# Kernel tuning notes

Hardware: AMD Instinct MI355X
Metric: run time of the kernel (lower is better)

The kernel has to match this reference:

```python
import jax, jax.numpy as jnp
import numpy as np
import math

N, S, R = 1, 128, 256
CM, CZ, C, MSA_H, PAIR_H, CTM, FF = 256, 128, 32, 8, 4, 128, 4
SCALE = 1.0 / math.sqrt(C)


def _ln(x, w, b):
    m = jnp.mean(x, -1, keepdims=True)
    v = jnp.var(x, -1, keepdims=True)
    return (x - m) / jnp.sqrt(v + 1e-5) * w + b


def _gated_attn(x, gate_w, qkv_w, out_w, head, bias=None):
    # x: [n, s, r, cin]; attention over r within each (n, s, head)
    n, s, r, _ = x.shape
    gate = jax.nn.sigmoid(x @ gate_w).reshape(n, s, r, head, C)
    qkv = (x @ qkv_w).reshape(n, s, r, 3, head, C)
    q, k, v = qkv[..., 0, :, :], qkv[..., 1, :, :], qkv[..., 2, :, :]
    sim = jax.nn.softmax(jnp.einsum('nsqhc,nskhc->nshqk', q, k) * SCALE, axis=-1)
    if bias is not None:
        sim = sim + bias  # NOTE: source adds bias AFTER softmax; kept faithful
    att = jnp.einsum('nshqk,nskhc->nsqhc', sim, v) * gate
    return att.reshape(n, s, r, head * C) @ out_w


def _tri_mul(x, n1w, n1b, n2w, n2b, p1, p2, p3, p4, p5, p6, incoming):
    xn = _ln(x, n1w, n1b)
    a = jax.nn.sigmoid(xn @ p1) * (xn @ p2)
    b = jax.nn.sigmoid(xn @ p3) * (xn @ p4)
    if incoming:
        p = jnp.einsum('nrsk,nrtk->nstk', a, b)
        g = jnp.swapaxes(jax.nn.sigmoid(xn @ p6), 1, 2)
    else:
        p = jnp.einsum('nsrk,ntrk->nstk', a, b)
        g = jax.nn.sigmoid(xn @ p6)
    return (_ln(p, n2w, n2b) @ p5) * g


def setup_inputs() -> dict:
    keys = iter(jax.random.split(jax.random.key(0), 80))

    def rn(shape, scale=0.02):
        return jax.random.normal(next(keys), shape, dtype=jnp.float32) * scale

    ones = lambda n: jnp.ones((n,), jnp.float32)
    zeros = lambda n: jnp.zeros((n,), jnp.float32)
    d = dict(
        msa_repr=rn((N, S, R, CM), 1.0),
        pair_repr=rn((N, R, R, CZ), 1.0),
        row_norm_m_w=ones(CM), row_norm_m_b=zeros(CM),
        row_norm_z_w=ones(CZ), row_norm_z_b=zeros(CZ),
        row_gate=rn((CM, MSA_H * C)), row_qkv=rn((CM, 3 * MSA_H * C)),
        row_out=rn((MSA_H * C, CM)), row_bias=rn((CZ, MSA_H)),
        col_norm_w=ones(CM), col_norm_b=zeros(CM),
        col_gate=rn((CM, MSA_H * C)), col_qkv=rn((CM, 3 * MSA_H * C)),
        col_out=rn((MSA_H * C, CM)),
        mt_norm_w=ones(CM), mt_norm_b=zeros(CM),
        mt_p1=rn((CM, FF * CM)), mt_p2=rn((FF * CM, CM)),
        outer_norm_w=ones(CM), outer_norm_b=zeros(CM),
        outer_p1=rn((CM, C)), outer_p2=rn((CM, C)), outer_out=rn((C * C, CZ)),
        tmo_n1_w=ones(CZ), tmo_n1_b=zeros(CZ), tmo_n2_w=ones(CTM), tmo_n2_b=zeros(CTM),
        tmo_p1=rn((CZ, CTM)), tmo_p2=rn((CZ, CTM)), tmo_p3=rn((CZ, CTM)), tmo_p4=rn((CZ, CTM)),
        tmo_p5=rn((CTM, CZ)), tmo_p6=rn((CZ, CZ)),
        tmi_n1_w=ones(CZ), tmi_n1_b=zeros(CZ), tmi_n2_w=ones(CTM), tmi_n2_b=zeros(CTM),
        tmi_p1=rn((CZ, CTM)), tmi_p2=rn((CZ, CTM)), tmi_p3=rn((CZ, CTM)), tmi_p4=rn((CZ, CTM)),
        tmi_p5=rn((CTM, CZ)), tmi_p6=rn((CZ, CZ)),
        tas_norm_w=ones(CZ), tas_norm_b=zeros(CZ),
        tas_gate=rn((CZ, PAIR_H * C)), tas_qkv=rn((CZ, 3 * PAIR_H * C)),
        tas_out=rn((PAIR_H * C, CZ)), tas_bias=rn((CZ, PAIR_H)),
        tae_norm_w=ones(CZ), tae_norm_b=zeros(CZ),
        tae_gate=rn((CZ, PAIR_H * C)), tae_qkv=rn((CZ, 3 * PAIR_H * C)),
        tae_out=rn((PAIR_H * C, CZ)), tae_bias=rn((CZ, PAIR_H)),
        pt_norm_w=ones(CZ), pt_norm_b=zeros(CZ),
        pt_p1=rn((CZ, FF * CZ)), pt_p2=rn((FF * CZ, CZ)),
    )
    return d


def reference(msa_repr, pair_repr, row_norm_m_w, row_norm_m_b, row_norm_z_w, row_norm_z_b, row_gate, row_qkv, row_out, row_bias, col_norm_w, col_norm_b, col_gate, col_qkv, col_out, mt_norm_w, mt_norm_b, mt_p1, mt_p2, outer_norm_w, outer_norm_b, outer_p1, outer_p2, outer_out, tmo_n1_w, tmo_n1_b, tmo_n2_w, tmo_n2_b, tmo_p1, tmo_p2, tmo_p3, tmo_p4, tmo_p5, tmo_p6, tmi_n1_w, tmi_n1_b, tmi_n2_w, tmi_n2_b, tmi_p1, tmi_p2, tmi_p3, tmi_p4, tmi_p5, tmi_p6, tas_norm_w, tas_norm_b, tas_gate, tas_qkv, tas_out, tas_bias, tae_norm_w, tae_norm_b, tae_gate, tae_qkv, tae_out, tae_bias, pt_norm_w, pt_norm_b, pt_p1, pt_p2):
    msa, pair = msa_repr, pair_repr
    # 1. MSA row attention with pair bias
    xm = _ln(msa, row_norm_m_w, row_norm_m_b)
    xz = _ln(pair, row_norm_z_w, row_norm_z_b)
    bias = jnp.transpose(xz @ row_bias, (0, 3, 1, 2))[:, None]  # [N,1,H,R,R]
    msa = msa + _gated_attn(xm, row_gate, row_qkv, row_out, MSA_H, bias)
    # 2. MSA column attention
    xm = _ln(msa, col_norm_w, col_norm_b)
    msa = msa + jnp.swapaxes(_gated_attn(jnp.swapaxes(xm, 1, 2), col_gate, col_qkv, col_out, MSA_H), 1, 2)
    # 3. MSA transition
    xm = _ln(msa, mt_norm_w, mt_norm_b)
    msa = msa + jax.nn.relu(xm @ mt_p1) @ mt_p2
    # 4. outer product mean (no division in source; sum over s)
    xm = _ln(msa, outer_norm_w, outer_norm_b)
    a = jnp.swapaxes(xm @ outer_p1, 1, 2)  # [n,r,s,c]
    b = jnp.swapaxes(xm @ outer_p2, 1, 2)  # [n,t,s,c]
    outer = jnp.einsum('nrsc,ntse->nrtce', a, b).reshape(a.shape[0], a.shape[1], b.shape[1], C * C)
    pair = pair + outer @ outer_out
    # 5/6. triangle multiplicative updates (outgoing then incoming)
    pair = pair + _tri_mul(pair, tmo_n1_w, tmo_n1_b, tmo_n2_w, tmo_n2_b, tmo_p1, tmo_p2, tmo_p3, tmo_p4, tmo_p5, tmo_p6, False)
    pair = pair + _tri_mul(pair, tmi_n1_w, tmi_n1_b, tmi_n2_w, tmi_n2_b, tmi_p1, tmi_p2, tmi_p3, tmi_p4, tmi_p5, tmi_p6, True)
    # 7. triangle attention (node start)
    xz = _ln(pair, tas_norm_w, tas_norm_b)
    bias = jnp.transpose(xz @ tas_bias, (0, 1, 3, 2))[:, :, :, None, :]  # [N,S,H,1,R]
    pair = pair + _gated_attn(xz, tas_gate, tas_qkv, tas_out, PAIR_H, bias)
    # 8. triangle attention (node end): transpose residue axes
    xz = jnp.swapaxes(_ln(pair, tae_norm_w, tae_norm_b), 1, 2)
    bias = jnp.transpose(xz @ tae_bias, (0, 1, 3, 2))[:, :, :, None, :]
    pair = pair + jnp.swapaxes(_gated_attn(xz, tae_gate, tae_qkv, tae_out, PAIR_H, bias), 1, 2)
    # 9. pair transition
    xz = _ln(pair, pt_norm_w, pt_norm_b)
    pair = pair + jax.nn.relu(xz @ pt_p1) @ pt_p2
    return msa, pair
```

## Files before the change

kernel.cpp:

```cpp
#include <hip/hip_runtime.h>
#include <hip/hip_bf16.h>
#include <stdint.h>

typedef __hip_bfloat16 bf16;
typedef __attribute__((ext_vector_type(4))) int   i32x4;
typedef __attribute__((ext_vector_type(4))) float f32x4;


__device__ __forceinline__ float toF(float x){ return x; }
__device__ __forceinline__ float toF(bf16 x){ return __bfloat162float(x); }
__device__ __forceinline__ bf16  toB(float x){ return __float2bfloat16(x); }

__device__ __forceinline__ void gload16(const bf16* g, bf16* l){
    __builtin_amdgcn_global_load_lds((const __attribute__((address_space(1))) void*)g,
                                     (__attribute__((address_space(3))) void*)l, 16, 0, 0);
}

#define NW_IN 58
struct WStage {
    const void* src[NW_IN];
    int off[NW_IN];
    int K[NW_IN], N[NW_IN];
};
__global__ __launch_bounds__(256) void cvt_all_k(WStage t, bf16* __restrict__ base,
                                                 const uint32_t* __restrict__ probe){
    bool isbf = (probe[0] == 0x3F803F80u);
    const int wi = blockIdx.y;
    const void* in = t.src[wi];
    bf16* out = base + t.off[wi];
    const int K = t.K[wi], N = t.N[wi];
    const int total = K ? K*N : N;
    for (int i = blockIdx.x*256 + threadIdx.x; i < total; i += gridDim.x*256){
        float v = isbf ? toF(((const bf16*)in)[i]) : ((const float*)in)[i];
        if (K){ int k = i / N, n = i - k*N; out[(size_t)n*K + k] = toB(v); }
        else    out[i] = toB(v);
    }
}
__global__ void in2f_k(const void* __restrict__ in, float* __restrict__ out, int n,
                       const uint32_t* __restrict__ probe){
    bool isbf = (probe[0] == 0x3F803F80u);
    int i = blockIdx.x*256 + threadIdx.x;
    if (i < n) out[i] = isbf ? toF(((const bf16*)in)[i]) : ((const float*)in)[i];
}

template<typename T>
__global__ void ln_k(const T* __restrict__ x, const bf16* __restrict__ w, const bf16* __restrict__ b,
                     bf16* __restrict__ out, int D){
    int row = blockIdx.x, c = threadIdx.x;
    float v = toF(x[(size_t)row*D + c]);
    float s1 = v, s2 = v*v;
    #pragma unroll
    for (int o=32;o>0;o>>=1){ s1 += __shfl_down(s1,o); s2 += __shfl_down(s2,o); }
    __shared__ float r1[4], r2[4];
    int lane = c & 63, wid = c >> 6;
    if (lane==0){ r1[wid]=s1; r2[wid]=s2; }
    __syncthreads();
    int nw = blockDim.x >> 6;
    float m=0.f, q=0.f;
    for (int i=0;i<nw;i++){ m+=r1[i]; q+=r2[i]; }
    m /= (float)D; q = q/(float)D - m*m;
    float inv = rsqrtf(q + 1e-5f);
    out[(size_t)row*D + c] = toB((v-m)*inv*toF(w[c]) + toF(b[c]));
}

template<int MODE, int HN>
__global__ __launch_bounds__(256) void bproj_k(const bf16* __restrict__ xz, const bf16* __restrict__ Wb,
                                               float* __restrict__ outb){
    __shared__ float WbS[128*HN];
    const int i = blockIdx.x, t = threadIdx.x;
    for (int idx = t; idx < 128*HN; idx += 256) WbS[idx] = toF(Wb[idx]);
    __syncthreads();
    const bf16* row = xz + ((size_t)i*256 + t)*128;
    float d[HN] = {};
    #pragma unroll 4
    for (int c8 = 0; c8 < 16; ++c8){
        uint4 v = *(const uint4*)(row + c8*8);
        bf16 tmp[8]; *(uint4*)tmp = v;
        #pragma unroll
        for (int u=0;u<8;u++){
            float x = toF(tmp[u]);
            #pragma unroll
            for (int h=0;h<HN;h++) d[h] += x * WbS[(c8*8+u)*HN + h];
        }
    }
    #pragma unroll
    for (int h=0;h<HN;h++){
        size_t idx = (MODE==0) ? ((size_t)h*65536 + (size_t)i*256 + t)
                   : (MODE==1) ? ((size_t)(i*HN+h)*256 + t)
                               : ((size_t)(t*HN+h)*256 + i);
        outb[idx] = d[h];
    }
}

template<int ACT, int MUL, int RES>
__global__ __launch_bounds__(256) void mgemm_k(const bf16* __restrict__ A, const bf16* __restrict__ Bt,
                                               bf16* __restrict__ C, float* __restrict__ Res,
                                               const bf16* __restrict__ Mul,
                                               int M, int N, int K, int lda, int ldbt, int ldc,
                                               int res_off, int gtrans){
    __shared__ alignas(16) bf16 As[128*32];
    __shared__ alignas(16) bf16 Bs[128*32];
    const int tid  = threadIdx.x;
    const int m0   = blockIdx.y << 7, n0 = blockIdx.x << 7;
    const int lane = tid & 63, w = tid >> 6;
    const int wr   = (w >> 1) << 6, wc = (w & 1) << 6;
    const int fr   = lane & 15, fq = lane >> 4;
    const int sr = tid >> 2, sc = (tid & 3) << 3;
    const bf16* ga = A  + (size_t)(m0 + sr)*lda  + sc;
    const bf16* gb = Bt + (size_t)(n0 + sr)*ldbt + sc;
    bf16* la = As + tid*8;
    bf16* lb = Bs + tid*8;
    const size_t gaS = (size_t)64*lda, gbS = (size_t)64*ldbt;

    f32x4 acc[4][4] = {};
    for (int k0=0; k0<K; k0+=32){
        gload16(ga, la);        gload16(ga + gaS, la + 2048);
        gload16(gb, lb);        gload16(gb + gbS, lb + 2048);
        ga += 32; gb += 32;
        __syncthreads();
        i32x4 af[4], bv[4];
        #pragma unroll
        for (int i=0;i<4;i++) af[i] = *(const i32x4*)(As + ((wr + i*16 + fr) << 5) + (fq << 3));
        #pragma unroll
        for (int j=0;j<4;j++) bv[j] = *(const i32x4*)(Bs + ((wc + j*16 + fr) << 5) + (fq << 3));
        #pragma unroll
        for (int i=0;i<4;i++)
            #pragma unroll
            for (int j=0;j<4;j++)
                asm("v_mfma_f32_16x16x32_bf16 %0, %1, %2, %0"
                    : "+v"(acc[i][j]) : "v"(af[i]), "v"(bv[j]));
        __syncthreads();
    }
    #pragma unroll
    for (int i=0;i<4;i++){
        const int mB = m0 + wr + i*16 + (fq << 2);
        #pragma unroll
        for (int j=0;j<4;j++){
            const int n = n0 + wc + j*16 + fr;
            #pragma unroll
            for (int r=0;r<4;r++){
                int m = mB + r;
                float x = acc[i][j][r];
                if (ACT==1) x = 1.f/(1.f + __expf(-x));
                else if (ACT==2) x = fmaxf(x, 0.f);
                if (MUL){
                    int mr = gtrans ? (((m & 255) << 8) | (m >> 8)) : m;
                    x *= toF(Mul[(size_t)mr*N + n]);
                }
                if (RES) Res[(size_t)(m + res_off)*N + n] += x;
                else     C[(size_t)m*ldc + n] = toB(x);
            }
        }
    }
}

template<int ACT, int MUL, int RES, int GATE>
__global__ __launch_bounds__(256) void sgemm_k(const bf16* __restrict__ A,
        const bf16* __restrict__ Bt1, const bf16* __restrict__ Bt2,
        bf16* __restrict__ C, float* __restrict__ Res, const bf16* __restrict__ Mul,
        int M, int lda, int ldbt, int ldc, int ldmul, int res_off, int gtrans){
    __shared__ alignas(16) bf16 Bs1[128*128];
    __shared__ alignas(16) bf16 Bs2[GATE ? 128*128 : 16];
    const int tid = threadIdx.x;
    for (int idx = tid; idx < 2048; idx += 256){
        int n = idx >> 4, cc = idx & 15;
        int sc = (cc ^ (n & 15)) << 3;
        *(uint4*)(Bs1 + n*128 + sc) = *(const uint4*)(Bt1 + (size_t)n*ldbt + (cc<<3));
        if (GATE)
            *(uint4*)(Bs2 + n*128 + sc) = *(const uint4*)(Bt2 + (size_t)n*ldbt + (cc<<3));
    }
    __syncthreads();
    const int lane = tid & 63, w = tid >> 6;
    const int fr = lane & 15, fq = lane >> 4;
    const int mb = blockIdx.x*128 + w*32;
    f32x4 acc[2][8] = {};
    f32x4 acc2[2][8] = {};
    #pragma unroll
    for (int k0=0;k0<4;k0++){
        i32x4 af[2];
        #pragma unroll
        for (int i=0;i<2;i++)
            af[i] = *(const i32x4*)(A + (size_t)(mb + i*16 + fr)*lda + k0*32 + fq*8);
        const int co = ((k0*4 + fq) ^ fr) << 3;
        #pragma unroll
        for (int j=0;j<8;j++){
            i32x4 bf1 = *(const i32x4*)(Bs1 + (j*16+fr)*128 + co);
            #pragma unroll
            for (int i=0;i<2;i++)
                asm("v_mfma_f32_16x16x32_bf16 %0, %1, %2, %0"
                    : "+v"(acc[i][j]) : "v"(af[i]), "v"(bf1));
            if (GATE){
                i32x4 bf2 = *(const i32x4*)(Bs2 + (j*16+fr)*128 + co);
                #pragma unroll
                for (int i=0;i<2;i++)
                    asm("v_mfma_f32_16x16x32_bf16 %0, %1, %2, %0"
                        : "+v"(acc2[i][j]) : "v"(af[i]), "v"(bf2));
            }
        }
    }
    #pragma unroll
    for (int i=0;i<2;i++){
        #pragma unroll
        for (int j=0;j<8;j++){
            const int n = j*16 + fr;
            #pragma unroll
            for (int r=0;r<4;r++){
                int m = mb + i*16 + (fq<<2) + r;
                float x = acc[i][j][r];
                if (GATE) x = acc2[i][j][r] / (1.f + __expf(-x));
                else if (ACT==1) x = 1.f/(1.f + __expf(-x));
                else if (ACT==2) x = fmaxf(x, 0.f);
                if (MUL){
                    int mr = gtrans ? (((m & 255) << 8) | (m >> 8)) : m;
                    x *= toF(Mul[(size_t)mr*ldmul + n]);
                }
                if (RES) Res[(size_t)(m + res_off)*128 + n] += x;
                else     C[(size_t)m*ldc + n] = toB(x);
            }
        }
    }
}

__global__ __launch_bounds__(256) void btrimul_k(const bf16* __restrict__ aT, const bf16* __restrict__ bT,
                                                 bf16* __restrict__ pT){
    __shared__ alignas(16) bf16 As[128*32];
    __shared__ alignas(16) bf16 Bs[128*32];
    const int tid  = threadIdx.x;
    const int m0   = blockIdx.y << 7, n0 = blockIdx.x << 7;
    const size_t zb = (size_t)blockIdx.z << 16;
    const int lane = tid & 63, w = tid >> 6;
    const int wr   = (w >> 1) << 6, wc = (w & 1) << 6;
    const int fr   = lane & 15, fq = lane >> 4;
    const int sr = tid >> 2, sc = (tid & 3) << 3;
    const bf16* ga = aT + zb + (size_t)(m0 + sr)*256 + sc;
    const bf16* gb = bT + zb + (size_t)(n0 + sr)*256 + sc;
    bf16* la = As + tid*8;
    bf16* lb = Bs + tid*8;
    const size_t gS = (size_t)64*256;

    f32x4 acc[4][4] = {};
    for (int k0=0; k0<256; k0+=32){
        gload16(ga, la);        gload16(ga + gS, la + 2048);
        gload16(gb, lb);        gload16(gb + gS, lb + 2048);
        ga += 32; gb += 32;
        __syncthreads();
        i32x4 af[4], bv[4];
        #pragma unroll
        for (int i=0;i<4;i++) af[i] = *(const i32x4*)(As + ((wr + i*16 + fr) << 5) + (fq << 3));
        #pragma unroll
        for (int j=0;j<4;j++) bv[j] = *(const i32x4*)(Bs + ((wc + j*16 + fr) << 5) + (fq << 3));
        #pragma unroll
        for (int i=0;i<4;i++)
            #pragma unroll
            for (int j=0;j<4;j++)
                asm("v_mfma_f32_16x16x32_bf16 %0, %1, %2, %0"
                    : "+v"(acc[i][j]) : "v"(af[i]), "v"(bv[j]));
        __syncthreads();
    }
    #pragma unroll
    for (int i=0;i<4;i++){
        const int mB = m0 + wr + i*16 + (fq << 2);
        #pragma unroll
        for (int j=0;j<4;j++){
            const int n = n0 + wc + j*16 + fr;
            #pragma unroll
            for (int r=0;r<4;r++)
                pT[zb + (size_t)(mB + r)*256 + n] = toB(acc[i][j][r]);
        }
    }
}

__global__ __launch_bounds__(256) void rc2k_k(const bf16* __restrict__ in, bf16* __restrict__ out, int swap){
    __shared__ uint16_t T[128][137];
    const int tt = blockIdx.x, tid = threadIdx.x;
    size_t base_pp, out_off; int ppstride;
    if (!swap){ base_pp = (size_t)tt*128;                  ppstride = 1;   out_off = (size_t)tt*128; }
    else      { int J = tt>>1, I0 = (tt&1)*128;
                base_pp = (size_t)I0*256 + J;              ppstride = 256; out_off = (size_t)J*256 + I0; }
    for (int it=0; it<8; ++it){
        int idx = tid + it*256;
        int r = idx >> 4, c8 = (idx & 15) << 3;
        uint4 v = *(const uint4*)(in + (base_pp + (size_t)r*ppstride)*128 + c8);
        uint16_t tmp[8]; *(uint4*)tmp = v;
        #pragma unroll
        for (int t=0;t<8;t++) T[r][c8+t] = tmp[t];
    }
    __syncthreads();
    for (int it=0; it<8; ++it){
        int idx = tid + it*256;
        int k = idx >> 4, r8 = (idx & 15) << 3;
        uint16_t tmp[8];
        #pragma unroll
        for (int t=0;t<8;t++) tmp[t] = T[r8+t][k];
        *(uint4*)(out + (size_t)k*65536 + out_off + r8) = *(uint4*)tmp;
    }
}
__global__ __launch_bounds__(256) void k2rc_k(const bf16* __restrict__ in, bf16* __restrict__ out){
    __shared__ uint16_t T[128][137];
    const int tt = blockIdx.x, tid = threadIdx.x;
    const size_t a0 = (size_t)tt*128;
    for (int it=0; it<8; ++it){
        int idx = tid + it*256;
        int k = idx >> 4, r8 = (idx & 15) << 3;
        uint4 v = *(const uint4*)(in + (size_t)k*65536 + a0 + r8);
        uint16_t tmp[8]; *(uint4*)tmp = v;
        #pragma unroll
        for (int t=0;t<8;t++) T[r8+t][k] = tmp[t];
    }
    __syncthreads();
    for (int it=0; it<8; ++it){
        int idx = tid + it*256;
        int r = idx >> 4, c8 = (idx & 15) << 3;
        uint16_t tmp[8];
        #pragma unroll
        for (int t=0;t<8;t++) tmp[t] = T[r][c8+t];
        *(uint4*)(out + (a0 + r)*128 + c8) = *(uint4*)tmp;
    }
}

template<int ACT, int MUL, int RES>
__global__ __launch_bounds__(256) void gemm_k(const bf16* __restrict__ A, const bf16* __restrict__ Bw,
                                              bf16* __restrict__ C, float* __restrict__ Res,
                                              const bf16* __restrict__ Mul,
                                              int M, int N, int K, int ldb, int res_off, int gtrans){
    __shared__ float As[64][33];
    __shared__ float Bs[32][65];
    int tid = threadIdx.x;
    int m0 = blockIdx.y*64, n0 = blockIdx.x*64;
    int tx = tid & 15, ty = tid >> 4;
    float acc[4][4] = {};
    for (int k0=0; k0<K; k0+=32){
        for (int i=tid; i<64*32; i+=256){
            int r = i>>5, cc = i&31;
            As[r][cc] = toF(A[(size_t)(m0+r)*K + k0 + cc]);
        }
        for (int i=tid; i<32*64; i+=256){
            int r = i>>6, cc = i&63; int col = n0+cc;
            Bs[r][cc] = (col < N) ? toF(Bw[(size_t)(k0+r)*ldb + col]) : 0.f;
        }
        __syncthreads();
        #pragma unroll 8
        for (int k=0;k<32;k++){
            float a4[4], b4[4];
            #pragma unroll
            for (int i=0;i<4;i++) a4[i] = As[ty*4+i][k];
            #pragma unroll
            for (int j=0;j<4;j++) b4[j] = Bs[k][tx*4+j];
            #pragma unroll
            for (int i=0;i<4;i++)
                #pragma unroll
                for (int j=0;j<4;j++) acc[i][j] += a4[i]*b4[j];
        }
        __syncthreads();
    }
    #pragma unroll
    for (int i=0;i<4;i++){
        int m = m0 + ty*4 + i;
        #pragma unroll
        for (int j=0;j<4;j++){
            int n = n0 + tx*4 + j;
            if (n >= N) continue;
            float x = acc[i][j];
            if (ACT==1) x = 1.f/(1.f + __expf(-x));
            else if (ACT==2) x = fmaxf(x, 0.f);
            if (MUL){
                int mr = gtrans ? (((m & 255) << 8) | (m >> 8)) : m;
                x *= toF(Mul[(size_t)mr*N + n]);
            }
            if (RES) Res[(size_t)(m + res_off)*N + n] += x;
            else     C[(size_t)m*N + n] = toB(x);
        }
    }
}

template<int BIAS, int L>
__global__ __launch_bounds__(256) void attn4_k(bf16* __restrict__ QO,
                                               const bf16* __restrict__ Kp, const bf16* __restrict__ Vp,
                                               const float* __restrict__ bias,
                                               int H, int GN, int sO, int sL){
    constexpr int MW  = L/4;
    constexpr int IFR = MW/16;
    constexpr int KC  = 32;
    constexpr int NCH = L/KC;
    constexpr int VP  = L + 8;
    __shared__ alignas(16) bf16 VT_lds[32*VP];
    __shared__ alignas(16) bf16 P_lds[L*40];
    __shared__ float red[8*32 + 32];
    const int o = blockIdx.y, h = blockIdx.x, tid = threadIdx.x;
    const int lane = tid & 63, w = tid >> 6;
    const int fr = lane & 15, fq = lane >> 4;

    for (int idx = tid; idx < L*4; idx += 256){
        int l = idx >> 2, c8 = (idx & 3) << 3;
        size_t p = (size_t)(o*sO + l*sL)*GN + h*32 + c8;
        uint4 vv = *(const uint4*)(Vp + p);
        bf16 tmp[8]; *(uint4*)tmp = vv;
        #pragma unroll
        for (int t=0;t<8;t++) VT_lds[(c8+t)*VP + l] = tmp[t];
    }
    __syncthreads();

    float* ObS = red + 256;
    if (BIAS == 2){
        int c = tid & 31, g = tid >> 5;
        const float* bp = bias + (size_t)(o*H + h)*256;
        float p = 0.f;
        for (int k = g*(L/8); k < (g+1)*(L/8); ++k)
            p += bp[k] * toF(VT_lds[c*VP + k]);
        red[g*32 + c] = p;
        __syncthreads();
        if (tid < 32){
            float s = 0.f;
            #pragma unroll
            for (int g2=0; g2<8; ++g2) s += red[g2*32 + tid];
            ObS[tid] = s;
        }
        __syncthreads();
    }

    i32x4 qf[IFR];
    #pragma unroll
    for (int i=0;i<IFR;i++){
        int q = w*MW + i*16 + fr;
        qf[i] = *(const i32x4*)(QO + (size_t)(o*sO + q*sL)*GN + h*32 + fq*8);
    }
    const bf16* kbase = Kp + (size_t)o*sO*GN + h*32 + fq*8 + (size_t)fr*sL*GN;
    const size_t kstep = (size_t)sL*GN;

    bf16* Pw = P_lds + w*MW*40;
    f32x4 accO[IFR][2] = {};
    f32x4 accB[IFR][2] = {};
    float lsum[IFR][4] = {};

    for (int ch=0; ch<NCH; ++ch){
        const int k0 = ch*KC;
        f32x4 sa[IFR][2] = {};
        i32x4 kf[2];
        #pragma unroll
        for (int j=0;j<2;j++) kf[j] = *(const i32x4*)(kbase + (size_t)(k0 + j*16)*kstep);
        #pragma unroll
        for (int i=0;i<IFR;i++)
            #pragma unroll
            for (int j=0;j<2;j++)
                asm("v_mfma_f32_16x16x32_bf16 %0, %1, %2, %0"
                    : "+v"(sa[i][j]) : "v"(qf[i]), "v"(kf[j]));
        #pragma unroll
        for (int i=0;i<IFR;i++)
            #pragma unroll
            for (int j=0;j<2;j++)
                #pragma unroll
                for (int r=0;r<4;r++){
                    float e = __expf(sa[i][j][r] * 0.17677669529663687f);
                    lsum[i][r] += e;
                    Pw[(i*16 + fq*4 + r)*40 + j*16 + fr] = toB(e);
                }
        i32x4 vf[2];
        #pragma unroll
        for (int j=0;j<2;j++) vf[j] = *(const i32x4*)(VT_lds + (j*16 + fr)*VP + k0 + fq*8);
        #pragma unroll
        for (int i=0;i<IFR;i++){
            i32x4 pa = *(const i32x4*)(Pw + (i*16 + fr)*40 + fq*8);
            #pragma unroll
            for (int j=0;j<2;j++)
                asm("v_mfma_f32_16x16x32_bf16 %0, %1, %2, %0"
                    : "+v"(accO[i][j]) : "v"(pa), "v"(vf[j]));
        }
        if (BIAS == 1){
            #pragma unroll
            for (int it=0; it<32; ++it){
                int q = it*2 + (lane>>5), kk = lane&31;
                Pw[q*40 + kk] = toB(bias[(size_t)h*65536 + (size_t)(w*MW + q)*256 + k0 + kk]);
            }
            #pragma unroll
            for (int i=0;i<IFR;i++){
                i32x4 pa = *(const i32x4*)(Pw + (i*16 + fr)*40 + fq*8);
                #pragma unroll
                for (int j=0;j<2;j++)
                    asm("v_mfma_f32_16x16x32_bf16 %0, %1, %2, %0"
                        : "+v"(accB[i][j]) : "v"(pa), "v"(vf[j]));
            }
        }
    }
    #pragma unroll
    for (int i=0;i<IFR;i++)
        #pragma unroll
        for (int r=0;r<4;r++){
            float s = lsum[i][r];
            s += __shfl_xor(s, 1); s += __shfl_xor(s, 2);
            s += __shfl_xor(s, 4); s += __shfl_xor(s, 8);
            lsum[i][r] = 1.f / s;
        }
    #pragma unroll
    for (int i=0;i<IFR;i++)
        #pragma unroll
        for (int j=0;j<2;j++)
            #pragma unroll
            for (int r=0;r<4;r++){
                int q = w*MW + i*16 + fq*4 + r;
                int c = j*16 + fr;
                float v = accO[i][j][r]*lsum[i][r];
                if (BIAS==1) v += accB[i][j][r];
                if (BIAS==2) v += ObS[c];
                QO[(size_t)(o*sO + q*sL)*GN + h*32 + c] = toB(v);
            }
}

__global__ void mulsig2_k(bf16* __restrict__ a, int n){
    int i = blockIdx.x*256 + threadIdx.x;
    if (i < n){
        int m = i >> 8, c = i & 255;
        size_t o = (size_t)m*768 + c;
        float sg = 1.f/(1.f + __expf(-toF(a[o + 256])));
        a[o] = toB(toF(a[o]) * sg);
    }
}

__global__ __launch_bounds__(256) void outer_k(const bf16* __restrict__ ap, const bf16* __restrict__ bp,
                                               bf16* __restrict__ outc, int r0){
    int t = blockIdx.x, rl = blockIdx.y, r = r0 + rl;
    __shared__ float As[128*32], Bs[128*32];
    for (int idx=threadIdx.x; idx<128*32; idx+=256){
        int s = idx>>5, c = idx&31;
        As[idx] = toF(ap[((size_t)s*256 + r)*32 + c]);
        Bs[idx] = toF(bp[((size_t)s*256 + t)*32 + c]);
    }
    __syncthreads();
    int ce0 = threadIdx.x*4;
    int c = ce0 >> 5, e0 = ce0 & 31;
    float acc[4] = {0.f,0.f,0.f,0.f};
    for (int s=0;s<128;s++){
        float av = As[s*32 + c];
        #pragma unroll
        for (int j=0;j<4;j++) acc[j] += av*Bs[s*32 + e0 + j];
    }
    size_t row = (size_t)rl*256 + t;
    #pragma unroll
    for (int j=0;j<4;j++) outc[row*1024 + ce0 + j] = toB(acc[j]);
}

static bool tshape(int i, int& K, int& N){
    switch(i){
        case 6: case 8: case 12: case 14: K=256; N=256;  return true;
        case 7: case 13:                  K=256; N=768;  return true;
        case 17:                          K=256; N=1024; return true;
        case 18:                          K=1024;N=256;  return true;
        case 23:                          K=1024;N=128;  return true;
        case 47: case 53:                 K=128; N=384;  return true;
        case 58:                          K=128; N=512;  return true;
        case 59:                          K=512; N=128;  return true;
        default:
            if ((i>=28&&i<=33)||(i>=38&&i<=43)||i==46||i==48||i==52||i==54){ K=128; N=128; return true; }
            return false;
    }
}

extern "C" void kernel_launch(void* const* d_in, const int* in_sizes, int n_in,
                              void* d_out, int out_size, void* d_ws, size_t ws_size,
                              hipStream_t stream){
    (void)n_in; (void)out_size; (void)ws_size;
    const int MSA_N  = 128*256*256;
    const int PAIR_N = 256*256*128;
    const uint32_t* probe = (const uint32_t*)d_in[2];

    char*  w     = (char*)d_ws;
    bf16*  wsts  = (bf16*)(w);
    float* biasF = (float*)(w + 4194304);
    bf16*  lnb   = (bf16*)(w + 6291456);
    bf16*  bufA  = (bf16*)(w + 23068672);
    bf16*  bufB  = (bf16*)(w + 39845888);
    bf16*  bufC  = (bf16*)(w + 56623104);

    float* msaF  = (float*)d_out;
    float* pairF = msaF + MSA_N;

    size_t woff[64]; { size_t acc = 0;
        for (int i=2;i<60;i++){ woff[i] = acc; acc += ((size_t)in_sizes[i] + 63) & ~(size_t)63; } }
    #define W(i) (wsts + woff[i])

    {
        WStage st;
        for (int i=2;i<60;i++){
            int tk, tn;
            st.src[i-2] = d_in[i];
            st.off[i-2] = (int)woff[i];
            if (tshape(i, tk, tn)){ st.K[i-2]=tk; st.N[i-2]=tn; }
            else                   { st.K[i-2]=0;  st.N[i-2]=in_sizes[i]; }
        }
        cvt_all_k<<<dim3(64, NW_IN),256,0,stream>>>(st, wsts, probe);
    }

    in2f_k<<<32768,256,0,stream>>>(d_in[0], msaF,  MSA_N,  probe);
    in2f_k<<<32768,256,0,stream>>>(d_in[1], pairF, PAIR_N, probe);

    ln_k<float><<<32768,256,0,stream>>>(msaF, W(2), W(3), lnb, 256);
    ln_k<float><<<65536,128,0,stream>>>(pairF, W(4), W(5), bufC, 128);
    bproj_k<0,8><<<256,256,0,stream>>>(bufC, W(9), biasF);
    mgemm_k<0,0,0><<<dim3(6,256),256,0,stream>>>(lnb, W(7), bufA, nullptr, nullptr,
                                                 32768,768,256, 256,256,768, 0,0);
    attn4_k<1,256><<<dim3(8,128),256,0,stream>>>(bufA, bufA+256, bufA+512, biasF, 8, 768, 256, 1);
    mgemm_k<0,0,0><<<dim3(2,256),256,0,stream>>>(lnb, W(6), bufA+256, nullptr, nullptr,
                                                 32768,256,256, 256,256,768, 0,0);
    mulsig2_k<<<32768,256,0,stream>>>(bufA, MSA_N);
    mgemm_k<0,0,1><<<dim3(2,256),256,0,stream>>>(bufA, W(8), nullptr, msaF, nullptr,
                                                 32768,256,256, 768,256,256, 0,0);

    ln_k<float><<<32768,256,0,stream>>>(msaF, W(10), W(11), lnb, 256);
    mgemm_k<0,0,0><<<dim3(6,256),256,0,stream>>>(lnb, W(13), bufA, nullptr, nullptr,
                                                 32768,768,256, 256,256,768, 0,0);
    attn4_k<0,128><<<dim3(8,256),256,0,stream>>>(bufA, bufA+256, bufA+512, nullptr, 8, 768, 1, 256);
    mgemm_k<0,0,0><<<dim3(2,256),256,0,stream>>>(lnb, W(12), bufA+256, nullptr, nullptr,
                                                 32768,256,256, 256,256,768, 0,0);
    mulsig2_k<<<32768,256,0,stream>>>(bufA, MSA_N);
    mgemm_k<0,0,1><<<dim3(2,256),256,0,stream>>>(bufA, W(14), nullptr, msaF, nullptr,
                                                 32768,256,256, 768,256,256, 0,0);

    ln_k<float><<<32768,256,0,stream>>>(msaF, W(15), W(16), lnb, 256);
    for (int ch=0; ch<4; ++ch){
        mgemm_k<2,0,0><<<dim3(2,256),256,0,stream>>>(lnb, W(17)+ch*65536, bufA, nullptr, nullptr,
                                                     32768,256,256, 256,256,256, 0,0);
        mgemm_k<0,0,1><<<dim3(2,256),256,0,stream>>>(bufA, W(18)+ch*256, nullptr, msaF, nullptr,
                                                     32768,256,256, 256,1024,256, 0,0);
    }

    ln_k<float><<<32768,256,0,stream>>>(msaF, W(19), W(20), lnb, 256);
    gemm_k<0,0,0><<<dim3(1,512),256,0,stream>>>(lnb, W(21), bufA, nullptr, nullptr, 32768,32,256, 32, 0,0);
    gemm_k<0,0,0><<<dim3(1,512),256,0,stream>>>(lnb, W(22), bufB, nullptr, nullptr, 32768,32,256, 32, 0,0);
    for (int ch=0; ch<8; ++ch){
        outer_k<<<dim3(256,32),256,0,stream>>>(bufA, bufB, lnb, ch*32);
        mgemm_k<0,0,1><<<dim3(1,64),256,0,stream>>>(lnb, W(23), nullptr, pairF, nullptr,
                                                    8192,128,1024, 1024,1024,128, ch*8192,0);
    }

    for (int tm=0; tm<2; ++tm){
        int o = tm ? 34 : 24;
        int inc = tm;
        ln_k<float><<<65536,128,0,stream>>>(pairF, W(o+0), W(o+1), lnb, 128);
        sgemm_k<0,0,0,1><<<512,256,0,stream>>>(lnb, W(o+4), W(o+5), bufA, nullptr, nullptr,
                                               65536, 128,128,128,0, 0,0);
        sgemm_k<0,0,0,1><<<512,256,0,stream>>>(lnb, W(o+6), W(o+7), bufB, nullptr, nullptr,
                                               65536, 128,128,128,0, 0,0);
        rc2k_k<<<512,256,0,stream>>>(bufA, bufC, inc);
        rc2k_k<<<512,256,0,stream>>>(bufB, bufA, inc);
        btrimul_k<<<dim3(2,2,128),256,0,stream>>>(bufC, bufA, bufB);
        k2rc_k<<<512,256,0,stream>>>(bufB, bufC);
        ln_k<bf16><<<65536,128,0,stream>>>(bufC, W(o+2), W(o+3), bufC, 128);
        sgemm_k<1,0,0,0><<<512,256,0,stream>>>(lnb, W(o+9), nullptr, bufA, nullptr, nullptr,
                                               65536, 128,128,128,0, 0,0);
        sgemm_k<0,1,1,0><<<512,256,0,stream>>>(bufC, W(o+8), nullptr, nullptr, pairF, bufA,
                                               65536, 128,128,0,128, 0, inc);
    }

    ln_k<float><<<65536,128,0,stream>>>(pairF, W(44), W(45), lnb, 128);
    bproj_k<1,4><<<256,256,0,stream>>>(lnb, W(49), biasF);
    mgemm_k<0,0,0><<<dim3(3,512),256,0,stream>>>(lnb, W(47), bufA, nullptr, nullptr,
                                                 65536,384,128, 128,128,384, 0,0);
    attn4_k<2,256><<<dim3(4,256),256,0,stream>>>(bufA, bufA+128, bufA+256, biasF, 4, 384, 256, 1);
    sgemm_k<1,1,0,0><<<512,256,0,stream>>>(lnb, W(46), nullptr, bufA+128, nullptr, bufA,
                                           65536, 128,128,384,384, 0,0);
    sgemm_k<0,0,1,0><<<512,256,0,stream>>>(bufA+128, W(48), nullptr, nullptr, pairF, nullptr,
                                           65536, 384,128,0,0, 0,0);
    ln_k<float><<<65536,128,0,stream>>>(pairF, W(50), W(51), lnb, 128);
    bproj_k<2,4><<<256,256,0,stream>>>(lnb, W(55), biasF);
    mgemm_k<0,0,0><<<dim3(3,512),256,0,stream>>>(lnb, W(53), bufA, nullptr, nullptr,
                                                 65536,384,128, 128,128,384, 0,0);
    attn4_k<2,256><<<dim3(4,256),256,0,stream>>>(bufA, bufA+128, bufA+256, biasF, 4, 384, 1, 256);
    sgemm_k<1,1,0,0><<<512,256,0,stream>>>(lnb, W(52), nullptr, bufA+128, nullptr, bufA,
                                           65536, 128,128,384,384, 0,0);
    sgemm_k<0,0,1,0><<<512,256,0,stream>>>(bufA+128, W(54), nullptr, nullptr, pairF, nullptr,
                                           65536, 384,128,0,0, 0,0);

    ln_k<float><<<65536,128,0,stream>>>(pairF, W(56), W(57), lnb, 128);
    for (int ch=0; ch<4; ++ch){
        sgemm_k<2,0,0,0><<<512,256,0,stream>>>(lnb, W(58)+ch*16384, nullptr, bufA, nullptr, nullptr,
                                               65536, 128,128,128,0, 0,0);
        sgemm_k<0,0,1,0><<<512,256,0,stream>>>(bufA, W(59)+ch*128, nullptr, nullptr, pairF, nullptr,
                                               65536, 128,512,0,0, 0,0);
    }
}
```

Baseline: 2.499 ms.

## Store QKV projections head-major so attention reads contiguous per-head slabs

```diff
diff --git a/kernel.cpp b/kernel.cpp
--- a/kernel.cpp
+++ b/kernel.cpp
@@ -92,12 +92,12 @@
     }
 }
 
-template<int ACT, int MUL, int RES>
+template<int ACT, int MUL, int RES, int HM>
 __global__ __launch_bounds__(256) void mgemm_k(const bf16* __restrict__ A, const bf16* __restrict__ Bt,
                                                bf16* __restrict__ C, float* __restrict__ Res,
                                                const bf16* __restrict__ Mul,
-                                               int M, int N, int K, int lda, int ldbt, int ldc,
-                                               int res_off, int gtrans){
+                                               int M, int N, int K, int lda, size_t astep,
+                                               int ldbt, size_t ldc, int res_off, int gtrans){
     __shared__ alignas(16) bf16 As[128*32];
     __shared__ alignas(16) bf16 Bs[128*32];
     const int tid  = threadIdx.x;
@@ -116,7 +116,7 @@
     for (int k0=0; k0<K; k0+=32){
         gload16(ga, la);        gload16(ga + gaS, la + 2048);
         gload16(gb, lb);        gload16(gb + gbS, lb + 2048);
-        ga += 32; gb += 32;
+        ga += astep; gb += 32;
         __syncthreads();
         i32x4 af[4], bv[4];
         #pragma unroll
@@ -148,17 +148,18 @@
                     x *= toF(Mul[(size_t)mr*N + n]);
                 }
                 if (RES) Res[(size_t)(m + res_off)*N + n] += x;
+                else if (HM) C[(size_t)(n>>5)*ldc + (size_t)m*32 + (n&31)] = toB(x);
                 else     C[(size_t)m*ldc + n] = toB(x);
             }
         }
     }
 }
 
-template<int ACT, int MUL, int RES, int GATE>
+template<int ACT, int MUL, int RES, int GATE, int MHM>
 __global__ __launch_bounds__(256) void sgemm_k(const bf16* __restrict__ A,
         const bf16* __restrict__ Bt1, const bf16* __restrict__ Bt2,
         bf16* __restrict__ C, float* __restrict__ Res, const bf16* __restrict__ Mul,
-        int M, int lda, int ldbt, int ldc, int ldmul, int res_off, int gtrans){
+        int M, int lda, int ldbt, int ldc, size_t ldmul, int res_off, int gtrans){
     __shared__ alignas(16) bf16 Bs1[128*128];
     __shared__ alignas(16) bf16 Bs2[GATE ? 128*128 : 16];
     const int tid = threadIdx.x;
@@ -212,7 +213,8 @@
                 else if (ACT==2) x = fmaxf(x, 0.f);
                 if (MUL){
                     int mr = gtrans ? (((m & 255) << 8) | (m >> 8)) : m;
-                    x *= toF(Mul[(size_t)mr*ldmul + n]);
+                    if (MHM) x *= toF(Mul[(size_t)(n>>5)*ldmul + (size_t)mr*32 + (n&31)]);
+                    else     x *= toF(Mul[(size_t)mr*ldmul + n]);
                 }
                 if (RES) Res[(size_t)(m + res_off)*128 + n] += x;
                 else     C[(size_t)m*ldc + n] = toB(x);
@@ -377,7 +379,7 @@
 __global__ __launch_bounds__(256) void attn4_k(bf16* __restrict__ QO,
                                                const bf16* __restrict__ Kp, const bf16* __restrict__ Vp,
                                                const float* __restrict__ bias,
-                                               int H, int GN, int sO, int sL){
+                                               int H, size_t HS, int sO, int sL){
     constexpr int MW  = L/4;
     constexpr int IFR = MW/16;
     constexpr int KC  = 32;
@@ -389,10 +391,11 @@
     const int o = blockIdx.y, h = blockIdx.x, tid = threadIdx.x;
     const int lane = tid & 63, w = tid >> 6;
     const int fr = lane & 15, fq = lane >> 4;
+    const size_t hb = (size_t)h*HS;
 
     for (int idx = tid; idx < L*4; idx += 256){
         int l = idx >> 2, c8 = (idx & 3) << 3;
-        size_t p = (size_t)(o*sO + l*sL)*GN + h*32 + c8;
+        size_t p = hb + (size_t)(o*sO + l*sL)*32 + c8;
         uint4 vv = *(const uint4*)(Vp + p);
         bf16 tmp[8]; *(uint4*)tmp = vv;
         #pragma unroll
@@ -422,10 +425,10 @@
     #pragma unroll
     for (int i=0;i<IFR;i++){
         int q = w*MW + i*16 + fr;
-        qf[i] = *(const i32x4*)(QO + (size_t)(o*sO + q*sL)*GN + h*32 + fq*8);
-    }
-    const bf16* kbase = Kp + (size_t)o*sO*GN + h*32 + fq*8 + (size_t)fr*sL*GN;
-    const size_t kstep = (size_t)sL*GN;
+        qf[i] = *(const i32x4*)(QO + hb + (size_t)(o*sO + q*sL)*32 + fq*8);
+    }
+    const bf16* kbase = Kp + hb + (size_t)o*sO*32 + fq*8 + (size_t)fr*sL*32;
+    const size_t kstep = (size_t)sL*32;
 
     bf16* Pw = P_lds + w*MW*40;
     f32x4 accO[IFR][2] = {};
@@ -501,16 +504,17 @@
                 float v = accO[i][j][r]*lsum[i][r];
                 if (BIAS==1) v += accB[i][j][r];
                 if (BIAS==2) v += ObS[c];
-                QO[(size_t)(o*sO + q*sL)*GN + h*32 + c] = toB(v);
+                QO[hb + (size_t)(o*sO + q*sL)*32 + c] = toB(v);
             }
 }
 
-__global__ void mulsig2_k(bf16* __restrict__ a, int n){
+__global__ void mulsigHM_k(bf16* __restrict__ a, const bf16* __restrict__ g, size_t HS, int NC, int n){
     int i = blockIdx.x*256 + threadIdx.x;
     if (i < n){
-        int m = i >> 8, c = i & 255;
-        size_t o = (size_t)m*768 + c;
-        float sg = 1.f/(1.f + __expf(-toF(a[o + 256])));
+        int m = i / NC, col = i - m*NC;
+        int h = col >> 5, c = col & 31;
+        size_t o = (size_t)h*HS + (size_t)m*32 + c;
+        float sg = 1.f/(1.f + __expf(-toF(g[(size_t)m*NC + col])));
         a[o] = toB(toF(a[o]) * sg);
     }
 }
@@ -560,6 +564,8 @@
     (void)n_in; (void)out_size; (void)ws_size;
     const int MSA_N  = 128*256*256;
     const int PAIR_N = 256*256*128;
+    const size_t HSm = (size_t)32768*32;
+    const size_t HSp = (size_t)65536*32;
     const uint32_t* probe = (const uint32_t*)d_in[2];
 
     char*  w     = (char*)d_ws;
@@ -595,31 +601,31 @@
     ln_k<float><<<32768,256,0,stream>>>(msaF, W(2), W(3), lnb, 256);
     ln_k<float><<<65536,128,0,stream>>>(pairF, W(4), W(5), bufC, 128);
     bproj_k<0,8><<<256,256,0,stream>>>(bufC, W(9), biasF);
-    mgemm_k<0,0,0><<<dim3(6,256),256,0,stream>>>(lnb, W(7), bufA, nullptr, nullptr,
-                                                 32768,768,256, 256,256,768, 0,0);
-    attn4_k<1,256><<<dim3(8,128),256,0,stream>>>(bufA, bufA+256, bufA+512, biasF, 8, 768, 256, 1);
-    mgemm_k<0,0,0><<<dim3(2,256),256,0,stream>>>(lnb, W(6), bufA+256, nullptr, nullptr,
-                                                 32768,256,256, 256,256,768, 0,0);
-    mulsig2_k<<<32768,256,0,stream>>>(bufA, MSA_N);
-    mgemm_k<0,0,1><<<dim3(2,256),256,0,stream>>>(bufA, W(8), nullptr, msaF, nullptr,
-                                                 32768,256,256, 768,256,256, 0,0);
+    mgemm_k<0,0,0,1><<<dim3(6,256),256,0,stream>>>(lnb, W(7), bufA, nullptr, nullptr,
+                                                   32768,768,256, 256,32,256, HSm, 0,0);
+    attn4_k<1,256><<<dim3(8,128),256,0,stream>>>(bufA, bufA+8*HSm, bufA+16*HSm, biasF, 8, HSm, 256, 1);
+    mgemm_k<0,0,0,0><<<dim3(2,256),256,0,stream>>>(lnb, W(6), bufA+8*HSm, nullptr, nullptr,
+                                                   32768,256,256, 256,32,256, 256, 0,0);
+    mulsigHM_k<<<32768,256,0,stream>>>(bufA, bufA+8*HSm, HSm, 256, MSA_N);
+    mgemm_k<0,0,1,0><<<dim3(2,256),256,0,stream>>>(bufA, W(8), nullptr, msaF, nullptr,
+                                                   32768,256,256, 32,HSm,256, 256, 0,0);
 
     ln_k<float><<<32768,256,0,stream>>>(msaF, W(10), W(11), lnb, 256);
-    mgemm_k<0,0,0><<<dim3(6,256),256,0,stream>>>(lnb, W(13), bufA, nullptr, nullptr,
-                                                 32768,768,256, 256,256,768, 0,0);
-    attn4_k<0,128><<<dim3(8,256),256,0,stream>>>(bufA, bufA+256, bufA+512, nullptr, 8, 768, 1, 256);
-    mgemm_k<0,0,0><<<dim3(2,256),256,0,stream>>>(lnb, W(12), bufA+256, nullptr, nullptr,
-                                                 32768,256,256, 256,256,768, 0,0);
-    mulsig2_k<<<32768,256,0,stream>>>(bufA, MSA_N);
-    mgemm_k<0,0,1><<<dim3(2,256),256,0,stream>>>(bufA, W(14), nullptr, msaF, nullptr,
-                                                 32768,256,256, 768,256,256, 0,0);
+    mgemm_k<0,0,0,1><<<dim3(6,256),256,0,stream>>>(lnb, W(13), bufA, nullptr, nullptr,
+                                                   32768,768,256, 256,32,256, HSm, 0,0);
+    attn4_k<0,128><<<dim3(8,256),256,0,stream>>>(bufA, bufA+8*HSm, bufA+16*HSm, nullptr, 8, HSm, 1, 256);
+    mgemm_k<0,0,0,0><<<dim3(2,256),256,0,stream>>>(lnb, W(12), bufA+8*HSm, nullptr, nullptr,
+                                                   32768,256,256, 256,32,256, 256, 0,0);
+    mulsigHM_k<<<32768,256,0,stream>>>(bufA, bufA+8*HSm, HSm, 256, MSA_N);
+    mgemm_k<0,0,1,0><<<dim3(2,256),256,0,stream>>>(bufA, W(14), nullptr, msaF, nullptr,
+                                                   32768,256,256, 32,HSm,256, 256, 0,0);
 
     ln_k<float><<<32768,256,0,stream>>>(msaF, W(15), W(16), lnb, 256);
     for (int ch=0; ch<4; ++ch){
-        mgemm_k<2,0,0><<<dim3(2,256),256,0,stream>>>(lnb, W(17)+ch*65536, bufA, nullptr, nullptr,
-                                                     32768,256,256, 256,256,256, 0,0);
-        mgemm_k<0,0,1><<<dim3(2,256),256,0,stream>>>(bufA, W(18)+ch*256, nullptr, msaF, nullptr,
-                                                     32768,256,256, 256,1024,256, 0,0);
+        mgemm_k<2,0,0,0><<<dim3(2,256),256,0,stream>>>(lnb, W(17)+ch*65536, bufA, nullptr, nullptr,
+                                                       32768,256,256, 256,32,256, 256, 0,0);
+        mgemm_k<0,0,1,0><<<dim3(2,256),256,0,stream>>>(bufA, W(18)+ch*256, nullptr, msaF, nullptr,
+                                                       32768,256,256, 256,32,1024, 256, 0,0);
     }
 
     ln_k<float><<<32768,256,0,stream>>>(msaF, W(19), W(20), lnb, 256);
@@ -627,53 +633,53 @@
     gemm_k<0,0,0><<<dim3(1,512),256,0,stream>>>(lnb, W(22), bufB, nullptr, nullptr, 32768,32,256, 32, 0,0);
     for (int ch=0; ch<8; ++ch){
         outer_k<<<dim3(256,32),256,0,stream>>>(bufA, bufB, lnb, ch*32);
-        mgemm_k<0,0,1><<<dim3(1,64),256,0,stream>>>(lnb, W(23), nullptr, pairF, nullptr,
-                                                    8192,128,1024, 1024,1024,128, ch*8192,0);
+        mgemm_k<0,0,1,0><<<dim3(1,64),256,0,stream>>>(lnb, W(23), nullptr, pairF, nullptr,
+                                                      8192,128,1024, 1024,32,1024, 128, ch*8192,0);
     }
 
     for (int tm=0; tm<2; ++tm){
         int o = tm ? 34 : 24;
         int inc = tm;
         ln_k<float><<<65536,128,0,stream>>>(pairF, W(o+0), W(o+1), lnb, 128);
-        sgemm_k<0,0,0,1><<<512,256,0,stream>>>(lnb, W(o+4), W(o+5), bufA, nullptr, nullptr,
-                                               65536, 128,128,128,0, 0,0);
-        sgemm_k<0,0,0,1><<<512,256,0,stream>>>(lnb, W(o+6), W(o+7), bufB, nullptr, nullptr,
-                                               65536, 128,128,128,0, 0,0);
+        sgemm_k<0,0,0,1,0><<<512,256,0,stream>>>(lnb, W(o+4), W(o+5), bufA, nullptr, nullptr,
+                                                 65536, 128,128,128,0, 0,0);
+        sgemm_k<0,0,0,1,0><<<512,256,0,stream>>>(lnb, W(o+6), W(o+7), bufB, nullptr, nullptr,
+                                                 65536, 128,128,128,0, 0,0);
         rc2k_k<<<512,256,0,stream>>>(bufA, bufC, inc);
         rc2k_k<<<512,256,0,stream>>>(bufB, bufA, inc);
         btrimul_k<<<dim3(2,2,128),256,0,stream>>>(bufC, bufA, bufB);
         k2rc_k<<<512,256,0,stream>>>(bufB, bufC);
         ln_k<bf16><<<65536,128,0,stream>>>(bufC, W(o+2), W(o+3), bufC, 128);
-        sgemm_k<1,0,0,0><<<512,256,0,stream>>>(lnb, W(o+9), nullptr, bufA, nullptr, nullptr,
-                                               65536, 128,128,128,0, 0,0);
-        sgemm_k<0,1,1,0><<<512,256,0,stream>>>(bufC, W(o+8), nullptr, nullptr, pairF, bufA,
-                                               65536, 128,128,0,128, 0, inc);
+        sgemm_k<1,0,0,0,0><<<512,256,0,stream>>>(lnb, W(o+9), nullptr, bufA, nullptr, nullptr,
+                                                 65536, 128,128,128,0, 0,0);
+        sgemm_k<0,1,1,0,0><<<512,256,0,stream>>>(bufC, W(o+8), nullptr, nullptr, pairF, bufA,
+                                                 65536, 128,128,0,128, 0, inc);
     }
 
     ln_k<float><<<65536,128,0,stream>>>(pairF, W(44), W(45), lnb, 128);
     bproj_k<1,4><<<256,256,0,stream>>>(lnb, W(49), biasF);
-    mgemm_k<0,0,0><<<dim3(3,512),256,0,stream>>>(lnb, W(47), bufA, nullptr, nullptr,
-                                                 65536,384,128, 128,128,384, 0,0);
-    attn4_k<2,256><<<dim3(4,256),256,0,stream>>>(bufA, bufA+128, bufA+256, biasF, 4, 384, 256, 1);
-    sgemm_k<1,1,0,0><<<512,256,0,stream>>>(lnb, W(46), nullptr, bufA+128, nullptr, bufA,
-                                           65536, 128,128,384,384, 0,0);
-    sgemm_k<0,0,1,0><<<512,256,0,stream>>>(bufA+128, W(48), nullptr, nullptr, pairF, nullptr,
-                                           65536, 384,128,0,0, 0,0);
+    mgemm_k<0,0,0,1><<<dim3(3,512),256,0,stream>>>(lnb, W(47), bufA, nullptr, nullptr,
+                                                   65536,384,128, 128,32,128, HSp, 0,0);
+    attn4_k<2,256><<<dim3(4,256),256,0,stream>>>(bufA, bufA+4*HSp, bufA+8*HSp, biasF, 4, HSp, 256, 1);
+    sgemm_k<1,1,0,0,1><<<512,256,0,stream>>>(lnb, W(46), nullptr, bufA+4*HSp, nullptr, bufA,
+                                             65536, 128,128,128, HSp, 0,0);
+    sgemm_k<0,0,1,0,0><<<512,256,0,stream>>>(bufA+4*HSp, W(48), nullptr, nullptr, pairF, nullptr,
+                                             65536, 128,128,0,0, 0,0);
     ln_k<float><<<65536,128,0,stream>>>(pairF, W(50), W(51), lnb, 128);
     bproj_k<2,4><<<256,256,0,stream>>>(lnb, W(55), biasF);
-    mgemm_k<0,0,0><<<dim3(3,512),256,0,stream>>>(lnb, W(53), bufA, nullptr, nullptr,
-                                                 65536,384,128, 128,128,384, 0,0);
-    attn4_k<2,256><<<dim3(4,256),256,0,stream>>>(bufA, bufA+128, bufA+256, biasF, 4, 384, 1, 256);
-    sgemm_k<1,1,0,0><<<512,256,0,stream>>>(lnb, W(52), nullptr, bufA+128, nullptr, bufA,
-                                           65536, 128,128,384,384, 0,0);
-    sgemm_k<0,0,1,0><<<512,256,0,stream>>>(bufA+128, W(54), nullptr, nullptr, pairF, nullptr,
-                                           65536, 384,128,0,0, 0,0);
+    mgemm_k<0,0,0,1><<<dim3(3,512),256,0,stream>>>(lnb, W(53), bufA, nullptr, nullptr,
+                                                   65536,384,128, 128,32,128, HSp, 0,0);
+    attn4_k<2,256><<<dim3(4,256),256,0,stream>>>(bufA, bufA+4*HSp, bufA+8*HSp, biasF, 4, HSp, 1, 256);
+    sgemm_k<1,1,0,0,1><<<512,256,0,stream>>>(lnb, W(52), nullptr, bufA+4*HSp, nullptr, bufA,
+                                             65536, 128,128,128, HSp, 0,0);
+    sgemm_k<0,0,1,0,0><<<512,256,0,stream>>>(bufA+4*HSp, W(54), nullptr, nullptr, pairF, nullptr,
+                                             65536, 128,128,0,0, 0,0);
 
     ln_k<float><<<65536,128,0,stream>>>(pairF, W(56), W(57), lnb, 128);
     for (int ch=0; ch<4; ++ch){
-        sgemm_k<2,0,0,0><<<512,256,0,stream>>>(lnb, W(58)+ch*16384, nullptr, bufA, nullptr, nullptr,
-                                               65536, 128,128,128,0, 0,0);
-        sgemm_k<0,0,1,0><<<512,256,0,stream>>>(bufA, W(59)+ch*128, nullptr, nullptr, pairF, nullptr,
-                                               65536, 128,512,0,0, 0,0);
-    }
-}
+        sgemm_k<2,0,0,0,0><<<512,256,0,stream>>>(lnb, W(58)+ch*16384, nullptr, bufA, nullptr, nullptr,
+                                                 65536, 128,128,128,0, 0,0);
+        sgemm_k<0,0,1,0,0><<<512,256,0,stream>>>(bufA, W(59)+ch*128, nullptr, nullptr, pairF, nullptr,
+                                                 65536, 128,512,0,0, 0,0);
+    }
+}
```

Measured after the change: 2.481 ms. About the same (-0.7%).
